# Optimization experiments

Hardware: AMD Instinct MI355X
Metric: run time of the kernel (lower is better)

The kernel has to match this reference:

```python
import jax, jax.numpy as jnp
import numpy as np
import math

N_G = 8
N_D = 5
N_SKEL = 50000
N_LINES = 200000
N_FACES = 200000
COS_PHI = 6.123233995736766e-17          # math.cos(math.pi/2), used for p12/p13 offsets
C90 = float(np.cos(np.float32(math.pi / 2)))  # torch float32 cos(pi/2) ~ -4.371e-08 (RotateMatrix)
S90 = float(np.sin(np.float32(math.pi / 2)))  # == 1.0


def _normalize(x):
    return x / jnp.linalg.norm(x, axis=-1, keepdims=True)


def setup_inputs() -> dict:
    key = jax.random.key(0)
    k1, k2, k3, k4, k5, k6, k7 = jax.random.split(key, 7)
    pos = jax.random.normal(k1, (N_SKEL, 3), dtype=jnp.float32)
    rad = jax.random.uniform(k2, (N_SKEL, 1), minval=0.5, maxval=1.5, dtype=jnp.float32)
    skel_xyzr = jnp.concatenate([pos, rad], axis=-1)
    # lines: two distinct skeleton indices per line
    base_l = jax.random.randint(k3, (N_LINES,), 0, N_SKEL, dtype=jnp.int32)
    off_l = 1 + jax.random.randint(k4, (N_LINES,), 0, N_SKEL - 1, dtype=jnp.int32)
    lines = jnp.stack([base_l, (base_l + off_l) % N_SKEL], axis=-1)
    # faces: three pairwise-distinct skeleton indices per face
    base_f = jax.random.randint(k5, (N_FACES,), 0, N_SKEL, dtype=jnp.int32)
    r1 = jax.random.randint(k6, (N_FACES,), 0, N_SKEL - 1, dtype=jnp.int32)
    r2 = jax.random.randint(k7, (N_FACES,), 0, N_SKEL - 2, dtype=jnp.int32)
    o1 = 1 + r1 % (N_SKEL - 1)
    o2 = 1 + (r1 + 1 + r2 % (N_SKEL - 2)) % (N_SKEL - 1)  # o2 != o1, both in [1, N-1]
    faces = jnp.stack([base_f, (base_f + o1) % N_SKEL, (base_f + o2) % N_SKEL], axis=-1)
    return {"skel_xyzr": skel_xyzr, "lines": lines, "faces": faces}


def _lines_points(skel_xyzr, lines):
    v1 = skel_xyzr[lines[:, 0], :3]   # [L,3]
    v2 = skel_xyzr[lines[:, 1], :3]
    r1 = skel_xyzr[lines[:, 0], 3]    # [L]
    r2 = skel_xyzr[lines[:, 1], 3]
    c12 = v2 - v1                      # [L,3] rotation axis (unnormalized)
    # PerpendicularVector: [1, 1, (-cx - cy)/cz]
    ones = jnp.ones_like(c12[:, 0])
    perp = jnp.stack([ones, ones, (-c12[:, 0] - c12[:, 1]) / c12[:, 2]], axis=-1)
    d0 = _normalize(perp)              # [L,3]
    axis = _normalize(c12)             # [L,3] unit axis (RotationMatrix normalizes)
    angles = (2.0 * jnp.pi / N_G) * jnp.arange(N_G, dtype=jnp.float32)  # [G]
    cosA = jnp.cos(angles)[None, :, None]
    sinA = jnp.sin(angles)[None, :, None]
    # Rodrigues rotation of d0 about axis, batched over angles: [L,G,3]
    kxd = jnp.cross(axis, d0)[:, None, :]
    kdd = (axis * jnp.sum(axis * d0, axis=-1, keepdims=True))[:, None, :]
    rot = d0[:, None, :] * cosA + kxd * sinA + kdd * (1.0 - cosA)
    nor = _normalize(rot)              # [L,G,3]
    p1 = v1[:, None, :] + nor * r1[:, None, None]  # [L,G,3]
    p2 = v2[:, None, :] + nor * r2[:, None, None]
    fr = jnp.arange(1, N_D, dtype=jnp.float32) / N_D  # [N_D-1]
    interp = p1[:, :, None, :] + (p2 - p1)[:, :, None, :] * fr[None, None, :, None]
    blk = jnp.concatenate([p1[:, :, None, :], p2[:, :, None, :], interp], axis=2)  # [L,G,N_D+1,3]
    return blk.reshape(-1, 3)


def _cone_intersect(va, ra, vb, vc, nrm):
    # intersect_point_of_cones, batched over faces
    cab = vb - va
    cac = vc - va
    pab = va + _normalize(cab) * (COS_PHI * ra)[:, None]
    pac = va + _normalize(cac) * (COS_PHI * ra)[:, None]
    u, v, w = cab[:, 0], cab[:, 1], cab[:, 2]  # unnormalized axis (as in RotateMatrix)
    c, s = C90, S90
    t = 1.0 - c
    d0 = (u * u + (v * v + w * w) * c) * nrm[:, 0] + (u * v * t - w * s) * nrm[:, 1] + (u * w * t + v * s) * nrm[:, 2]
    d1 = (u * v * t + w * s) * nrm[:, 0] + (v * v + (u * u + w * w) * c) * nrm[:, 1] + (v * w * t - u * s) * nrm[:, 2]
    d2 = (u * w * t - v * s) * nrm[:, 0] + (v * w * t + u * s) * nrm[:, 1] + (w * w + (u * u + v * v) * c) * nrm[:, 2]
    dir12 = jnp.stack([d0, d1, d2], axis=-1)  # [F,3]
    tt = jnp.sum((pac - pab) * cac, axis=-1) / jnp.sum(dir12 * cac, axis=-1)
    ip = pab + dir12 * tt[:, None]
    vap = ip - va
    sn = jnp.sqrt(ra * ra - jnp.sum(vap * vap, axis=-1))[:, None] * nrm
    return ip, sn


def _faces_points(skel_xyzr, faces):
    v1 = skel_xyzr[faces[:, 0], :3]
    v2 = skel_xyzr[faces[:, 1], :3]
    v3 = skel_xyzr[faces[:, 2], :3]
    r1 = skel_xyzr[faces[:, 0], 3]
    r2 = skel_xyzr[faces[:, 1], 3]
    r3 = skel_xyzr[faces[:, 2], 3]
    nrm = _normalize(jnp.cross(v1 - v2, v1 - v3))  # [F,3]
    ip1, sn1 = _cone_intersect(v1, r1, v2, v3, nrm)
    ip2, sn2 = _cone_intersect(v2, r2, v1, v3, nrm)
    ip3, sn3 = _cone_intersect(v3, r3, v1, v2, nrm)
    pf = jnp.stack([ip1 + sn1, ip2 + sn2, ip3 + sn3, ip1 - sn1, ip2 - sn2, ip3 - sn3], axis=1)  # [F,6,3]
    bar = jnp.stack([pf[:, 0:3].mean(axis=1), pf[:, 3:6].mean(axis=1)], axis=1)  # [F,2,3]
    return jnp.concatenate([pf.reshape(-1, 3), bar.reshape(-1, 3)], axis=0)


def reference(skel_xyzr, lines, faces):
    pts_lines = _lines_points(skel_xyzr, lines)   # [L*(n_d+1)*n_g, 3]
    pts_faces = _faces_points(skel_xyzr, faces)   # [F*6 + F*2, 3]
    return jnp.concatenate([pts_lines, pts_faces], axis=0)
```

## Files before the change

### kernel.cpp

```cpp
#include <hip/hip_runtime.h>
#include <math.h>

#define NG 8
#define NLINES 200000
#define NFACES 200000
#define PF_BASE  28800000
#define BAR_BASE 32400000

__constant__ float2 c_cs[8] = {
  {  1.0f,            0.0f           },
  {  0.70710678f,     0.70710678f    },
  { -4.37113883e-08f, 1.0f           },
  { -0.70710678f,     0.70710678f    },
  { -1.0f,           -8.74227766e-08f},
  { -0.70710678f,    -0.70710678f    },
  {  1.19248806e-08f,-1.0f           },
  {  0.70710678f,    -0.70710678f    },
};
__constant__ float c_fr[4] = {0.2f, 0.4f, 0.6f, 0.8f};

__global__ __launch_bounds__(256) void lines_kernel(
    const float4* __restrict__ skel, const int2* __restrict__ lines,
    float* __restrict__ out)
{
  __shared__ float lds[256 * 18];
  const int tid = threadIdx.x;
  const int p   = blockIdx.x * 256 + tid;
  const int li  = p >> 3;
  const int g   = p & 7;

  int2 ln = lines[li];
  float4 s1 = skel[ln.x];
  float4 s2 = skel[ln.y];
  float r1 = s1.w, r2 = s2.w;

  float cx = s2.x - s1.x, cy = s2.y - s1.y, cz = s2.z - s1.z;
  float pz = (-cx - cy) / cz;
  float invp = 1.0f / sqrtf(2.0f + pz * pz);
  float d0x = invp, d0y = invp, d0z = pz * invp;
  float invc = 1.0f / sqrtf(cx * cx + cy * cy + cz * cz);
  float ax = cx * invc, ay = cy * invc, az = cz * invc;
  float kx = ay * d0z - az * d0y;
  float ky = az * d0x - ax * d0z;
  float kz = ax * d0y - ay * d0x;
  float dd = ax * d0x + ay * d0y + az * d0z;

  float2 cs = c_cs[g];
  float cA = cs.x, sA = cs.y, omc = 1.0f - cA;
  float rx = d0x * cA + kx * sA + (ax * dd) * omc;
  float ry = d0y * cA + ky * sA + (ay * dd) * omc;
  float rz = d0z * cA + kz * sA + (az * dd) * omc;
  float invr = 1.0f / sqrtf(rx * rx + ry * ry + rz * rz);
  float nx = rx * invr, ny = ry * invr, nz = rz * invr;

  float p1x = s1.x + nx * r1, p1y = s1.y + ny * r1, p1z = s1.z + nz * r1;
  float p2x = s2.x + nx * r2, p2y = s2.y + ny * r2, p2z = s2.z + nz * r2;

  float* L = &lds[tid * 18];
  L[0] = p1x; L[1] = p1y; L[2] = p1z;
  L[3] = p2x; L[4] = p2y; L[5] = p2z;
  float dx = p2x - p1x, dy = p2y - p1y, dz = p2z - p1z;
#pragma unroll
  for (int d = 0; d < 4; ++d) {
    float fr = c_fr[d];
    L[6 + 3 * d + 0] = p1x + dx * fr;
    L[6 + 3 * d + 1] = p1y + dy * fr;
    L[6 + 3 * d + 2] = p1z + dz * fr;
  }
  __syncthreads();

  const float4* lv = (const float4*)lds;
  float4* ov = (float4*)(out + (size_t)blockIdx.x * (256 * 18));
#pragma unroll
  for (int v = tid; v < 1152; v += 256) ov[v] = lv[v];
}

struct F3 { float x, y, z; };
__device__ __forceinline__ F3 sub3(F3 a, F3 b) { return {a.x - b.x, a.y - b.y, a.z - b.z}; }
__device__ __forceinline__ float dot3(F3 a, F3 b) { return a.x * b.x + a.y * b.y + a.z * b.z; }

__device__ __forceinline__ void cone_intersect(F3 va, float ra, F3 vb, F3 vc, F3 n,
                                               F3& ip, F3& sn)
{
  const float COS_PHI = 6.123234e-17f;
  const float c = -4.37113883e-08f;
  const float s = 1.0f;
  const float t = 1.0f - c;

  F3 cab = sub3(vb, va);
  F3 cac = sub3(vc, va);
  float invab = 1.0f / sqrtf(dot3(cab, cab));
  float invac = 1.0f / sqrtf(dot3(cac, cac));
  float cr = COS_PHI * ra;
  F3 pab = {va.x + cab.x * invab * cr, va.y + cab.y * invab * cr, va.z + cab.z * invab * cr};
  F3 pac = {va.x + cac.x * invac * cr, va.y + cac.y * invac * cr, va.z + cac.z * invac * cr};

  float u = cab.x, v = cab.y, w = cab.z;
  float d0 = (u * u + (v * v + w * w) * c) * n.x + (u * v * t - w * s) * n.y + (u * w * t + v * s) * n.z;
  float d1 = (u * v * t + w * s) * n.x + (v * v + (u * u + w * w) * c) * n.y + (v * w * t - u * s) * n.z;
  float d2 = (u * w * t - v * s) * n.x + (v * w * t + u * s) * n.y + (w * w + (u * u + v * v) * c) * n.z;
  F3 dir = {d0, d1, d2};

  F3 dpp = sub3(pac, pab);
  float tt = dot3(dpp, cac) / dot3(dir, cac);
  ip = {pab.x + dir.x * tt, pab.y + dir.y * tt, pab.z + dir.z * tt};
  F3 vap = sub3(ip, va);
  float snm = sqrtf(ra * ra - dot3(vap, vap));
  sn = {snm * n.x, snm * n.y, snm * n.z};
}

__global__ __launch_bounds__(256) void faces_kernel(
    const float4* __restrict__ skel, const int* __restrict__ faces,
    float* __restrict__ out)
{
  __shared__ float lds_pf[256 * 18];
  __shared__ float lds_bar[256 * 6];
  const int tid = threadIdx.x;
  const int f = blockIdx.x * 256 + tid;
  const int blk0 = blockIdx.x * 256;
  const int cnt = (NFACES - blk0) < 256 ? (NFACES - blk0) : 256;

  if (f < NFACES) {
    int i0 = faces[3 * f + 0], i1 = faces[3 * f + 1], i2 = faces[3 * f + 2];
    float4 s1 = skel[i0], s2 = skel[i1], s3 = skel[i2];
    F3 v1 = {s1.x, s1.y, s1.z}; float r1 = s1.w;
    F3 v2 = {s2.x, s2.y, s2.z}; float r2 = s2.w;
    F3 v3 = {s3.x, s3.y, s3.z}; float r3 = s3.w;

    F3 e1 = sub3(v1, v2);
    F3 e2 = sub3(v1, v3);
    F3 crx = {e1.y * e2.z - e1.z * e2.y, e1.z * e2.x - e1.x * e2.z, e1.x * e2.y - e1.y * e2.x};
    float invn = 1.0f / sqrtf(dot3(crx, crx));
    F3 nrm = {crx.x * invn, crx.y * invn, crx.z * invn};

    F3 ip1, sn1, ip2, sn2, ip3, sn3;
    cone_intersect(v1, r1, v2, v3, nrm, ip1, sn1);
    cone_intersect(v2, r2, v1, v3, nrm, ip2, sn2);
    cone_intersect(v3, r3, v1, v2, nrm, ip3, sn3);

    float* P = &lds_pf[tid * 18];
    P[0]  = ip1.x + sn1.x; P[1]  = ip1.y + sn1.y; P[2]  = ip1.z + sn1.z;
    P[3]  = ip2.x + sn2.x; P[4]  = ip2.y + sn2.y; P[5]  = ip2.z + sn2.z;
    P[6]  = ip3.x + sn3.x; P[7]  = ip3.y + sn3.y; P[8]  = ip3.z + sn3.z;
    P[9]  = ip1.x - sn1.x; P[10] = ip1.y - sn1.y; P[11] = ip1.z - sn1.z;
    P[12] = ip2.x - sn2.x; P[13] = ip2.y - sn2.y; P[14] = ip2.z - sn2.z;
    P[15] = ip3.x - sn3.x; P[16] = ip3.y - sn3.y; P[17] = ip3.z - sn3.z;

    float* B = &lds_bar[tid * 6];
    B[0] = (P[0] + P[3] + P[6]) / 3.0f;
    B[1] = (P[1] + P[4] + P[7]) / 3.0f;
    B[2] = (P[2] + P[5] + P[8]) / 3.0f;
    B[3] = (P[9]  + P[12] + P[15]) / 3.0f;
    B[4] = (P[10] + P[13] + P[16]) / 3.0f;
    B[5] = (P[11] + P[14] + P[17]) / 3.0f;
  }
  __syncthreads();

  {
    int nfl = cnt * 18;
    float* opf = out + PF_BASE + (size_t)blk0 * 18;
    const float4* lp = (const float4*)lds_pf;
    float4* op4 = (float4*)opf;
    int nv = nfl >> 2;
    for (int v = tid; v < nv; v += 256) op4[v] = lp[v];
    for (int v = (nv << 2) + tid; v < nfl; v += 256) opf[v] = lds_pf[v];
  }
  {
    int nfl = cnt * 6;
    float* ob = out + BAR_BASE + (size_t)blk0 * 6;
    const float4* lb = (const float4*)lds_bar;
    float4* ob4 = (float4*)ob;
    int nv = nfl >> 2;
    for (int v = tid; v < nv; v += 256) ob4[v] = lb[v];
    for (int v = (nv << 2) + tid; v < nfl; v += 256) ob[v] = lds_bar[v];
  }
}

extern "C" void kernel_launch(void* const* d_in, const int* in_sizes, int n_in,
                              void* d_out, int out_size, void* d_ws, size_t ws_size,
                              hipStream_t stream)
{
  const float4* skel  = (const float4*)d_in[0];
  const int2*   lines = (const int2*)d_in[1];
  const int*    faces = (const int*)d_in[2];
  float* out = (float*)d_out;

  lines_kernel<<<6250, 256, 0, stream>>>(skel, lines, out);
  faces_kernel<<<(NFACES + 255) / 256, 256, 0, stream>>>(skel, faces, out);
}
```

Baseline: 148.3 us.

## Fuse lines and faces kernels into one launch with fast math intrinsics

Merges the two launches into one grid: the first 782 blocks handle faces and the remaining blocks handle lines, with the heavier face blocks scheduled first. The face path now reuses a single LDS buffer for the point and barycenter staging, adding extra barriers. Divisions and sqrt calls are replaced with AMD hardware rcp/rsq/sqrt builtins, trading exact IEEE rounding for fewer instructions. The aim is to remove the launch gap and tail between kernels and cut ALU cost, at the risk of small numeric differences.

```diff
diff --git a/kernel.cpp b/kernel.cpp
--- a/kernel.cpp
+++ b/kernel.cpp
@@ -4,8 +4,14 @@
 #define NG 8
 #define NLINES 200000
 #define NFACES 200000
+#define NFACE_BLOCKS 782
+#define NLINE_BLOCKS 6250
 #define PF_BASE  28800000
 #define BAR_BASE 32400000
+
+__device__ __forceinline__ float frcp(float x)  { return __builtin_amdgcn_rcpf(x); }
+__device__ __forceinline__ float frsq(float x)  { return __builtin_amdgcn_rsqf(x); }
+__device__ __forceinline__ float fsqrt(float x) { return __builtin_amdgcn_sqrtf(x); }
 
 __constant__ float2 c_cs[8] = {
   {  1.0f,            0.0f           },
@@ -19,62 +25,6 @@
 };
 __constant__ float c_fr[4] = {0.2f, 0.4f, 0.6f, 0.8f};
 
-__global__ __launch_bounds__(256) void lines_kernel(
-    const float4* __restrict__ skel, const int2* __restrict__ lines,
-    float* __restrict__ out)
-{
-  __shared__ float lds[256 * 18];
-  const int tid = threadIdx.x;
-  const int p   = blockIdx.x * 256 + tid;
-  const int li  = p >> 3;
-  const int g   = p & 7;
-
-  int2 ln = lines[li];
-  float4 s1 = skel[ln.x];
-  float4 s2 = skel[ln.y];
-  float r1 = s1.w, r2 = s2.w;
-
-  float cx = s2.x - s1.x, cy = s2.y - s1.y, cz = s2.z - s1.z;
-  float pz = (-cx - cy) / cz;
-  float invp = 1.0f / sqrtf(2.0f + pz * pz);
-  float d0x = invp, d0y = invp, d0z = pz * invp;
-  float invc = 1.0f / sqrtf(cx * cx + cy * cy + cz * cz);
-  float ax = cx * invc, ay = cy * invc, az = cz * invc;
-  float kx = ay * d0z - az * d0y;
-  float ky = az * d0x - ax * d0z;
-  float kz = ax * d0y - ay * d0x;
-  float dd = ax * d0x + ay * d0y + az * d0z;
-
-  float2 cs = c_cs[g];
-  float cA = cs.x, sA = cs.y, omc = 1.0f - cA;
-  float rx = d0x * cA + kx * sA + (ax * dd) * omc;
-  float ry = d0y * cA + ky * sA + (ay * dd) * omc;
-  float rz = d0z * cA + kz * sA + (az * dd) * omc;
-  float invr = 1.0f / sqrtf(rx * rx + ry * ry + rz * rz);
-  float nx = rx * invr, ny = ry * invr, nz = rz * invr;
-
-  float p1x = s1.x + nx * r1, p1y = s1.y + ny * r1, p1z = s1.z + nz * r1;
-  float p2x = s2.x + nx * r2, p2y = s2.y + ny * r2, p2z = s2.z + nz * r2;
-
-  float* L = &lds[tid * 18];
-  L[0] = p1x; L[1] = p1y; L[2] = p1z;
-  L[3] = p2x; L[4] = p2y; L[5] = p2z;
-  float dx = p2x - p1x, dy = p2y - p1y, dz = p2z - p1z;
-#pragma unroll
-  for (int d = 0; d < 4; ++d) {
-    float fr = c_fr[d];
-    L[6 + 3 * d + 0] = p1x + dx * fr;
-    L[6 + 3 * d + 1] = p1y + dy * fr;
-    L[6 + 3 * d + 2] = p1z + dz * fr;
-  }
-  __syncthreads();
-
-  const float4* lv = (const float4*)lds;
-  float4* ov = (float4*)(out + (size_t)blockIdx.x * (256 * 18));
-#pragma unroll
-  for (int v = tid; v < 1152; v += 256) ov[v] = lv[v];
-}
-
 struct F3 { float x, y, z; };
 __device__ __forceinline__ F3 sub3(F3 a, F3 b) { return {a.x - b.x, a.y - b.y, a.z - b.z}; }
 __device__ __forceinline__ float dot3(F3 a, F3 b) { return a.x * b.x + a.y * b.y + a.z * b.z; }
@@ -89,8 +39,8 @@
 
   F3 cab = sub3(vb, va);
   F3 cac = sub3(vc, va);
-  float invab = 1.0f / sqrtf(dot3(cab, cab));
-  float invac = 1.0f / sqrtf(dot3(cac, cac));
+  float invab = frsq(dot3(cab, cab));
+  float invac = frsq(dot3(cac, cac));
   float cr = COS_PHI * ra;
   F3 pab = {va.x + cab.x * invab * cr, va.y + cab.y * invab * cr, va.z + cab.z * invab * cr};
   F3 pac = {va.x + cac.x * invac * cr, va.y + cac.y * invac * cr, va.z + cac.z * invac * cr};
@@ -102,77 +52,141 @@
   F3 dir = {d0, d1, d2};
 
   F3 dpp = sub3(pac, pab);
-  float tt = dot3(dpp, cac) / dot3(dir, cac);
+  float tt = dot3(dpp, cac) * frcp(dot3(dir, cac));
   ip = {pab.x + dir.x * tt, pab.y + dir.y * tt, pab.z + dir.z * tt};
   F3 vap = sub3(ip, va);
-  float snm = sqrtf(ra * ra - dot3(vap, vap));
+  float snm = fsqrt(ra * ra - dot3(vap, vap));
   sn = {snm * n.x, snm * n.y, snm * n.z};
 }
 
-__global__ __launch_bounds__(256) void faces_kernel(
-    const float4* __restrict__ skel, const int* __restrict__ faces,
-    float* __restrict__ out)
+__global__ __launch_bounds__(256) void fused_kernel(
+    const float4* __restrict__ skel, const int2* __restrict__ lines,
+    const int* __restrict__ faces, float* __restrict__ out)
 {
-  __shared__ float lds_pf[256 * 18];
-  __shared__ float lds_bar[256 * 6];
+  __shared__ float lds[256 * 18];
   const int tid = threadIdx.x;
-  const int f = blockIdx.x * 256 + tid;
-  const int blk0 = blockIdx.x * 256;
-  const int cnt = (NFACES - blk0) < 256 ? (NFACES - blk0) : 256;
-
-  if (f < NFACES) {
-    int i0 = faces[3 * f + 0], i1 = faces[3 * f + 1], i2 = faces[3 * f + 2];
-    float4 s1 = skel[i0], s2 = skel[i1], s3 = skel[i2];
-    F3 v1 = {s1.x, s1.y, s1.z}; float r1 = s1.w;
-    F3 v2 = {s2.x, s2.y, s2.z}; float r2 = s2.w;
-    F3 v3 = {s3.x, s3.y, s3.z}; float r3 = s3.w;
-
-    F3 e1 = sub3(v1, v2);
-    F3 e2 = sub3(v1, v3);
-    F3 crx = {e1.y * e2.z - e1.z * e2.y, e1.z * e2.x - e1.x * e2.z, e1.x * e2.y - e1.y * e2.x};
-    float invn = 1.0f / sqrtf(dot3(crx, crx));
-    F3 nrm = {crx.x * invn, crx.y * invn, crx.z * invn};
-
-    F3 ip1, sn1, ip2, sn2, ip3, sn3;
-    cone_intersect(v1, r1, v2, v3, nrm, ip1, sn1);
-    cone_intersect(v2, r2, v1, v3, nrm, ip2, sn2);
-    cone_intersect(v3, r3, v1, v2, nrm, ip3, sn3);
-
-    float* P = &lds_pf[tid * 18];
-    P[0]  = ip1.x + sn1.x; P[1]  = ip1.y + sn1.y; P[2]  = ip1.z + sn1.z;
-    P[3]  = ip2.x + sn2.x; P[4]  = ip2.y + sn2.y; P[5]  = ip2.z + sn2.z;
-    P[6]  = ip3.x + sn3.x; P[7]  = ip3.y + sn3.y; P[8]  = ip3.z + sn3.z;
-    P[9]  = ip1.x - sn1.x; P[10] = ip1.y - sn1.y; P[11] = ip1.z - sn1.z;
-    P[12] = ip2.x - sn2.x; P[13] = ip2.y - sn2.y; P[14] = ip2.z - sn2.z;
-    P[15] = ip3.x - sn3.x; P[16] = ip3.y - sn3.y; P[17] = ip3.z - sn3.z;
-
-    float* B = &lds_bar[tid * 6];
-    B[0] = (P[0] + P[3] + P[6]) / 3.0f;
-    B[1] = (P[1] + P[4] + P[7]) / 3.0f;
-    B[2] = (P[2] + P[5] + P[8]) / 3.0f;
-    B[3] = (P[9]  + P[12] + P[15]) / 3.0f;
-    B[4] = (P[10] + P[13] + P[16]) / 3.0f;
-    B[5] = (P[11] + P[14] + P[17]) / 3.0f;
-  }
-  __syncthreads();
-
-  {
-    int nfl = cnt * 18;
-    float* opf = out + PF_BASE + (size_t)blk0 * 18;
-    const float4* lp = (const float4*)lds_pf;
-    float4* op4 = (float4*)opf;
-    int nv = nfl >> 2;
-    for (int v = tid; v < nv; v += 256) op4[v] = lp[v];
-    for (int v = (nv << 2) + tid; v < nfl; v += 256) opf[v] = lds_pf[v];
-  }
-  {
-    int nfl = cnt * 6;
-    float* ob = out + BAR_BASE + (size_t)blk0 * 6;
-    const float4* lb = (const float4*)lds_bar;
-    float4* ob4 = (float4*)ob;
-    int nv = nfl >> 2;
-    for (int v = tid; v < nv; v += 256) ob4[v] = lb[v];
-    for (int v = (nv << 2) + tid; v < nfl; v += 256) ob[v] = lds_bar[v];
+
+  if (blockIdx.x >= NFACE_BLOCKS) {
+    const int lb = blockIdx.x - NFACE_BLOCKS;
+    const int p  = lb * 256 + tid;
+    const int li = p >> 3;
+    const int g  = p & 7;
+
+    int2 ln = lines[li];
+    float4 s1 = skel[ln.x];
+    float4 s2 = skel[ln.y];
+    float r1 = s1.w, r2 = s2.w;
+
+    float cx = s2.x - s1.x, cy = s2.y - s1.y, cz = s2.z - s1.z;
+    float pz = (-cx - cy) * frcp(cz);
+    float invp = frsq(2.0f + pz * pz);
+    float d0x = invp, d0y = invp, d0z = pz * invp;
+    float invc = frsq(cx * cx + cy * cy + cz * cz);
+    float ax = cx * invc, ay = cy * invc, az = cz * invc;
+    float kx = ay * d0z - az * d0y;
+    float ky = az * d0x - ax * d0z;
+    float kz = ax * d0y - ay * d0x;
+    float dd = ax * d0x + ay * d0y + az * d0z;
+
+    float2 cs = c_cs[g];
+    float cA = cs.x, sA = cs.y, omc = 1.0f - cA;
+    float rx = d0x * cA + kx * sA + (ax * dd) * omc;
+    float ry = d0y * cA + ky * sA + (ay * dd) * omc;
+    float rz = d0z * cA + kz * sA + (az * dd) * omc;
+    float invr = frsq(rx * rx + ry * ry + rz * rz);
+    float nx = rx * invr, ny = ry * invr, nz = rz * invr;
+
+    float p1x = s1.x + nx * r1, p1y = s1.y + ny * r1, p1z = s1.z + nz * r1;
+    float p2x = s2.x + nx * r2, p2y = s2.y + ny * r2, p2z = s2.z + nz * r2;
+
+    float* L = &lds[tid * 18];
+    L[0] = p1x; L[1] = p1y; L[2] = p1z;
+    L[3] = p2x; L[4] = p2y; L[5] = p2z;
+    float dx = p2x - p1x, dy = p2y - p1y, dz = p2z - p1z;
+#pragma unroll
+    for (int d = 0; d < 4; ++d) {
+      float fr = c_fr[d];
+      L[6 + 3 * d + 0] = p1x + dx * fr;
+      L[6 + 3 * d + 1] = p1y + dy * fr;
+      L[6 + 3 * d + 2] = p1z + dz * fr;
+    }
+    __syncthreads();
+
+    const float4* lv = (const float4*)lds;
+    float4* ov = (float4*)(out + (size_t)lb * (256 * 18));
+#pragma unroll
+    for (int v = tid; v < 1152; v += 256) ov[v] = lv[v];
+  } else {
+    const int blk0 = blockIdx.x * 256;
+    const int f = blk0 + tid;
+    const int cnt = (NFACES - blk0) < 256 ? (NFACES - blk0) : 256;
+
+    float b0 = 0, b1 = 0, b2 = 0, b3 = 0, b4 = 0, b5 = 0;
+    if (f < NFACES) {
+      int i0 = faces[3 * f + 0], i1 = faces[3 * f + 1], i2 = faces[3 * f + 2];
+      float4 s1 = skel[i0], s2 = skel[i1], s3 = skel[i2];
+      F3 v1 = {s1.x, s1.y, s1.z}; float r1 = s1.w;
+      F3 v2 = {s2.x, s2.y, s2.z}; float r2 = s2.w;
+      F3 v3 = {s3.x, s3.y, s3.z}; float r3 = s3.w;
+
+      F3 e1 = sub3(v1, v2);
+      F3 e2 = sub3(v1, v3);
+      F3 crx = {e1.y * e2.z - e1.z * e2.y, e1.z * e2.x - e1.x * e2.z, e1.x * e2.y - e1.y * e2.x};
+      float invn = frsq(dot3(crx, crx));
+      F3 nrm = {crx.x * invn, crx.y * invn, crx.z * invn};
+
+      F3 ip1, sn1, ip2, sn2, ip3, sn3;
+      cone_intersect(v1, r1, v2, v3, nrm, ip1, sn1);
+      cone_intersect(v2, r2, v1, v3, nrm, ip2, sn2);
+      cone_intersect(v3, r3, v1, v2, nrm, ip3, sn3);
+
+      float* P = &lds[tid * 18];
+      float q0  = ip1.x + sn1.x, q1  = ip1.y + sn1.y, q2  = ip1.z + sn1.z;
+      float q3  = ip2.x + sn2.x, q4  = ip2.y + sn2.y, q5  = ip2.z + sn2.z;
+      float q6  = ip3.x + sn3.x, q7  = ip3.y + sn3.y, q8  = ip3.z + sn3.z;
+      float q9  = ip1.x - sn1.x, q10 = ip1.y - sn1.y, q11 = ip1.z - sn1.z;
+      float q12 = ip2.x - sn2.x, q13 = ip2.y - sn2.y, q14 = ip2.z - sn2.z;
+      float q15 = ip3.x - sn3.x, q16 = ip3.y - sn3.y, q17 = ip3.z - sn3.z;
+      P[0]=q0; P[1]=q1; P[2]=q2; P[3]=q3; P[4]=q4; P[5]=q5;
+      P[6]=q6; P[7]=q7; P[8]=q8; P[9]=q9; P[10]=q10; P[11]=q11;
+      P[12]=q12; P[13]=q13; P[14]=q14; P[15]=q15; P[16]=q16; P[17]=q17;
+
+      const float third = 0.33333334f;
+      b0 = (q0 + q3 + q6) * third;
+      b1 = (q1 + q4 + q7) * third;
+      b2 = (q2 + q5 + q8) * third;
+      b3 = (q9 + q12 + q15) * third;
+      b4 = (q10 + q13 + q16) * third;
+      b5 = (q11 + q14 + q17) * third;
+    }
+    __syncthreads();
+
+    {
+      int nfl = cnt * 18;
+      float* opf = out + PF_BASE + (size_t)blk0 * 18;
+      const float4* lp = (const float4*)lds;
+      float4* op4 = (float4*)opf;
+      int nv = nfl >> 2;
+      for (int v = tid; v < nv; v += 256) op4[v] = lp[v];
+      for (int v = (nv << 2) + tid; v < nfl; v += 256) opf[v] = lds[v];
+    }
+    __syncthreads();
+
+    if (f < NFACES) {
+      float* B = &lds[tid * 6];
+      B[0] = b0; B[1] = b1; B[2] = b2; B[3] = b3; B[4] = b4; B[5] = b5;
+    }
+    __syncthreads();
+
+    {
+      int nfl = cnt * 6;
+      float* ob = out + BAR_BASE + (size_t)blk0 * 6;
+      const float4* lb4 = (const float4*)lds;
+      float4* ob4 = (float4*)ob;
+      int nv = nfl >> 2;
+      for (int v = tid; v < nv; v += 256) ob4[v] = lb4[v];
+      for (int v = (nv << 2) + tid; v < nfl; v += 256) ob[v] = lds[v];
+    }
   }
 }
 
@@ -185,6 +199,5 @@
   const int*    faces = (const int*)d_in[2];
   float* out = (float*)d_out;
 
-  lines_kernel<<<6250, 256, 0, stream>>>(skel, lines, out);
-  faces_kernel<<<(NFACES + 255) / 256, 256, 0, stream>>>(skel, faces, out);
+  fused_kernel<<<NFACE_BLOCKS + NLINE_BLOCKS, 256, 0, stream>>>(skel, lines, faces, out);
 }
```

Measured after the change: 146.0 us. Within noise of the previous version (-1.6%).
